# Kernel tuning notes

Hardware: AMD Instinct MI355X
Metric: run time of the kernel (lower is better)

## Reference

```python
import jax, jax.numpy as jnp
import numpy as np
import math

B, NB, NA, NC, D, E, H = 4, 2048, 1024, 1024, 1024, 8, 16
HD = D // H
TOP_K = 2
T_MAX = 1000.0
TAU_MIN, TAU_MAX = 0.5, 2.0
W_MIN, W_MAX = 0.1, 0.2
CAP_LO, CAP_HI = 0.5, 0.6
FLOOR = min(0.05, 0.15 / E)       # cfg.routing_floor property
ALPHA = min(FLOOR * E, 1.0)       # routing-floor interpolation weight
BIAS_COEFF = 0.01
EPS = 1e-8


def _layernorm(x, g, b, eps=1e-5):
    mu = x.mean(-1, keepdims=True)
    var = ((x - mu) ** 2).mean(-1, keepdims=True)
    return (x - mu) * jax.lax.rsqrt(var + eps) * g + b


def _forward(tokens_B, output_A, output_C, in_proj_w, in_proj_b, out_proj_w, out_proj_b,
             ln_g, ln_b, te_w1, te_b1, te_w2, te_b2,
             gate_w1, gate_b1, gate_w2, gate_b2, expert_bias, t):
    t_norm = t.astype(jnp.float32) / T_MAX                 # (B,)
    ctx_C = jax.lax.stop_gradient(output_C)                # stopgrad_C_to_B
    ctx_AC = jnp.concatenate([output_A, ctx_C], axis=1)    # (B, NA+NC, D)

    # --- cross attention (torch nn.MultiheadAttention, batch_first) ---
    wq, wk, wv = jnp.split(in_proj_w, 3, axis=0)
    bq, bk, bv = jnp.split(in_proj_b, 3)
    q = (tokens_B @ wq.T + bq).reshape(B, NB, H, HD)
    k = (ctx_AC @ wk.T + bk).reshape(B, NA + NC, H, HD)
    v = (ctx_AC @ wv.T + bv).reshape(B, NA + NC, H, HD)
    scores = jnp.einsum('bqhd,bkhd->bhqk', q, k) / math.sqrt(HD)
    attn = jax.nn.softmax(scores, axis=-1)
    ctx = jnp.einsum('bhqk,bkhd->bqhd', attn, v).reshape(B, NB, D)
    ctx_B = ctx @ out_proj_w.T + out_proj_b
    ctx_B = _layernorm(ctx_B + tokens_B, ln_g, ln_b)

    # --- sinusoidal timestep embedding + 2-layer MLP ---
    half = D // 2
    freq = jnp.exp(-math.log(10000.0) * jnp.arange(half, dtype=jnp.float32) / (half - 1))
    args = t.astype(jnp.float32)[:, None] * freq
    emb = jnp.concatenate([jnp.sin(args), jnp.cos(args)], axis=-1)   # (B, D)
    t_emb = jax.nn.silu(emb @ te_w1.T + te_b1) @ te_w2.T + te_b2     # (B, D)
    t_emb = jnp.broadcast_to(t_emb[:, None, :], (B, NB, D))

    # --- gate MLP + expert bias + temperature ---
    gate_in = jnp.concatenate([tokens_B, ctx_B, t_emb], axis=-1)     # (B, NB, 3D)
    logits = jax.nn.relu(gate_in @ gate_w1.T + gate_b1) @ gate_w2.T + gate_b2 + expert_bias
    tau = (TAU_MIN + (TAU_MAX - TAU_MIN) * t_norm)[:, None, None]
    probs = jax.nn.softmax(logits / tau, axis=-1)                    # (B, NB, E)

    # routing floor: interpolate toward uniform
    probs = (1.0 - ALPHA) * probs + ALPHA / E

    # shared expert injection: expert 0 gets scheduled weight w(t), rest renormalised
    w = (W_MIN + (W_MAX - W_MIN) * t_norm)[:, None, None]
    shared = jnp.maximum(probs[..., 0:1], w)
    others = probs[..., 1:]
    others = others / jnp.maximum(others.sum(-1, keepdims=True), EPS) * (1.0 - shared)
    probs = jnp.concatenate([shared, others], axis=-1)

    # top-k mask (keep top-k probs, zero the rest)
    vals, idx = jax.lax.top_k(probs, TOP_K)
    dispatch = (jax.nn.one_hot(idx, E, dtype=probs.dtype) * vals[..., None]).sum(-2)

    # token-level hard cap (torch.no_grad -> stop_gradient) with redistribution
    cap = (CAP_LO + (CAP_HI - CAP_LO) * t_norm)[:, None, None]
    excess = jax.nn.relu(dispatch - cap)
    capped = dispatch - excess
    headroom = jax.nn.relu(cap - capped)
    head_sum = jnp.maximum(headroom.sum(-1, keepdims=True), EPS)
    capped = capped + excess.sum(-1, keepdims=True) * (headroom / head_sum)
    dispatch = jax.lax.stop_gradient(capped)

    # batch-level utilisation penalty on specialists 1..E-1
    fair = NB / max(E - 1, 1)
    load = dispatch.sum(axis=1).mean(axis=0)                          # (E,)
    pen_excess = jax.nn.relu(load[1:] - fair * 1.5)
    bias_penalty = BIAS_COEFF * jnp.sum(pen_excess ** 2)

    combine = dispatch / (dispatch.sum(-1, keepdims=True) + EPS)
    return dispatch, combine, bias_penalty


def setup_inputs() -> dict:
    key = jax.random.key(0)
    ks = jax.random.split(key, 12)
    g = lambda k, sh: jax.random.normal(k, sh, jnp.float32) * 0.02
    return dict(
        tokens_B=jax.random.normal(ks[0], (B, NB, D), jnp.float32),
        output_A=jax.random.normal(ks[1], (B, NA, D), jnp.float32),
        output_C=jax.random.normal(ks[2], (B, NC, D), jnp.float32),
        t=jax.random.randint(ks[3], (B,), 0, 1000, jnp.int32),
        in_proj_w=g(ks[4], (3 * D, D)),
        in_proj_b=jnp.zeros((3 * D,), jnp.float32),
        out_proj_w=g(ks[5], (D, D)),
        out_proj_b=jnp.zeros((D,), jnp.float32),
        ln_g=jnp.ones((D,), jnp.float32),
        ln_b=jnp.zeros((D,), jnp.float32),
        te_w1=g(ks[6], (2 * D, D)),
        te_b1=jnp.zeros((2 * D,), jnp.float32),
        te_w2=g(ks[7], (D, 2 * D)),
        te_b2=jnp.zeros((D,), jnp.float32),
        gate_w1=g(ks[8], (D, 3 * D)),
        gate_b1=jnp.zeros((D,), jnp.float32),
        gate_w2=g(ks[9], (E, D)),
        gate_b2=jnp.zeros((E,), jnp.float32),
        expert_bias=jnp.zeros((E,), jnp.float32),
    )


def reference(tokens_B, output_A, output_C, t, in_proj_w, in_proj_b, out_proj_w, out_proj_b,
              ln_g, ln_b, te_w1, te_b1, te_w2, te_b2,
              gate_w1, gate_b1, gate_w2, gate_b2, expert_bias):
    return _forward(tokens_B, output_A, output_C, in_proj_w, in_proj_b, out_proj_w, out_proj_b,
                    ln_g, ln_b, te_w1, te_b1, te_w2, te_b2,
                    gate_w1, gate_b1, gate_w2, gate_b2, expert_bias, t)
```

## Files before the change

### kernel.cpp

```cpp
#include <hip/hip_runtime.h>
#include <math.h>


typedef __attribute__((ext_vector_type(8))) short short8;
typedef __attribute__((ext_vector_type(4))) float f32x4;
typedef __attribute__((ext_vector_type(4))) unsigned int u32x4;
typedef unsigned short u16;
typedef unsigned int u32;

__global__ void zero_k(double* p) {
    if (threadIdx.x < 8) p[threadIdx.x] = 0.0;
}

__device__ inline u16 bf_hi(float x) {
    u32 u = __float_as_uint(x);
    u += 0x7FFFu + ((u >> 16) & 1u);
    return (u16)(u >> 16);
}
__device__ inline u16 bf_lo(float x, u16 h) {
    float hf = __uint_as_float(((u32)h) << 16);
    return bf_hi(x - hf);
}
__device__ inline u32 pack_bf(float x) {
    u32 u = __float_as_uint(x);
    u32 hi = (u + (0x7FFFu + ((u >> 16) & 1u))) >> 16;
    float hf = __uint_as_float(hi << 16);
    float d = x - hf;
    u32 u2 = __float_as_uint(d);
    u32 lo = (u2 + (0x7FFFu + ((u2 >> 16) & 1u))) >> 16;
    return (hi << 16) | lo;
}

__device__ inline void pack2(float p0, float p1, u32& o0, u32& o1) {
    u32 h01, l01;
    asm("v_cvt_pk_bf16_f32 %0, %1, %2" : "=v"(h01) : "v"(p0), "v"(p1));
    float d0 = p0 - __uint_as_float(h01 << 16);
    float d1 = p1 - __uint_as_float(h01 & 0xffff0000u);
    asm("v_cvt_pk_bf16_f32 %0, %1, %2" : "=v"(l01) : "v"(d0), "v"(d1));
    o0 = __builtin_amdgcn_perm(h01, l01, 0x05040100u);
    o1 = __builtin_amdgcn_perm(h01, l01, 0x07060302u);
}

__global__ __launch_bounds__(256)
void split_k(const float* __restrict__ in, u16* __restrict__ hi,
             u16* __restrict__ lo, int n4) {
    int i = blockIdx.x * 256 + threadIdx.x;
    if (i >= n4) return;
    float4 x = ((const float4*)in)[i];
    ushort4 h, l;
    h.x = bf_hi(x.x); l.x = bf_lo(x.x, h.x);
    h.y = bf_hi(x.y); l.y = bf_lo(x.y, h.y);
    h.z = bf_hi(x.z); l.z = bf_lo(x.z, h.z);
    h.w = bf_hi(x.w); l.w = bf_lo(x.w, h.w);
    ((ushort4*)hi)[i] = h;
    ((ushort4*)lo)[i] = l;
}

__global__ void emb_k(const int* __restrict__ t, float* __restrict__ emb) {
    int b = blockIdx.x;
    int j = threadIdx.x;
    float x1 = (float)(-9.210340371976184) * (float)j;
    float x2 = x1 / 511.0f;
    float freq = (float)exp((double)x2);
    float tf = (float)t[b];
    float arg = tf * freq;
    emb[b * 1024 + j]       = (float)sin((double)arg);
    emb[b * 1024 + 512 + j] = (float)cos((double)arg);
}

__global__ void te_fc_k(const float* __restrict__ in, const float* __restrict__ W,
                        const float* __restrict__ bias, float* __restrict__ out,
                        int K, int N, int do_silu) {
    int b = blockIdx.x;
    int wv = threadIdx.x >> 6, lane = threadIdx.x & 63;
    const float* inb = in + (size_t)b * K;
    int n0 = blockIdx.y * 16 + wv * 4;
    for (int q = 0; q < 4; q++) {
        int n = n0 + q;
        const float* wr = W + (size_t)n * K;
        float acc = 0.f;
        for (int c = lane * 4; c < K; c += 256) {
            float4 a  = *(const float4*)(inb + c);
            float4 w4 = *(const float4*)(wr + c);
            acc += a.x * w4.x + a.y * w4.y + a.z * w4.z + a.w * w4.w;
        }
#pragma unroll
        for (int off = 1; off < 64; off <<= 1) acc += __shfl_xor(acc, off, 64);
        if (lane == 0) {
            float x = acc + bias[n];
            out[(size_t)b * N + n] = do_silu ? (x / (1.0f + expf(-x))) : x;
        }
    }
}

template<bool GATE, bool RELU, int OMODE>
__global__ __launch_bounds__(256, 2)
void bfgemm_k(const u16* __restrict__ A0h, const u16* __restrict__ A0l,
              const u16* __restrict__ A1h, const u16* __restrict__ A1l,
              const u16* __restrict__ A2h, const u16* __restrict__ A2l,
              const u16* __restrict__ Wh_g, const u16* __restrict__ Wl_g,
              const float* __restrict__ bias, float* __restrict__ C,
              u16* __restrict__ Chi, u16* __restrict__ Clo, int K, float scale)
{
    __shared__ u16 Ah[128 * 32];
    __shared__ u16 Al[128 * 32];
    __shared__ u16 Wh[128 * 32];
    __shared__ u16 Wl[128 * 32];
    const int tid = threadIdx.x;
    const int row0 = blockIdx.x * 128;
    const int col0 = blockIdx.y * 128;
    const int wv = tid >> 6;
    const int lane = tid & 63;
    const int wrow = (wv & 1) * 64;
    const int wcol = (wv >> 1) * 64;
    const int l15 = lane & 15, quad = lane >> 4;

    f32x4 acc[4][4];
#pragma unroll
    for (int i = 0; i < 4; i++)
#pragma unroll
        for (int j = 0; j < 4; j++)
            acc[i][j] = (f32x4){0.f, 0.f, 0.f, 0.f};

    const int ar0 = tid >> 2, ak0 = (tid & 3) * 8;
    const int ar1 = (tid + 256) >> 2, ak1 = ((tid + 256) & 3) * 8;

    for (int kc = 0; kc < K; kc += 32) {
        const u16* pAh = A0h;
        const u16* pAl = A0l;
        int kk = kc;
        int tembseg = 0;
        if (GATE) {
            int seg = kc >> 10;
            if (seg == 1) { pAh = A1h; pAl = A1l; }
            else if (seg == 2) { pAh = A2h; pAl = A2l; tembseg = 1; }
            kk = kc & 1023;
        }
        const int astr = GATE ? 1024 : K;
        int g0 = row0 + ar0, g1 = row0 + ar1;
        if (GATE && tembseg) { g0 >>= 11; g1 >>= 11; }
        uint4 vah0 = *(const uint4*)&pAh[(size_t)g0 * astr + kk + ak0];
        uint4 vah1 = *(const uint4*)&pAh[(size_t)g1 * astr + kk + ak1];
        uint4 val0 = *(const uint4*)&pAl[(size_t)g0 * astr + kk + ak0];
        uint4 val1 = *(const uint4*)&pAl[(size_t)g1 * astr + kk + ak1];
        uint4 vwh0 = *(const uint4*)&Wh_g[(size_t)(col0 + ar0) * K + kc + ak0];
        uint4 vwh1 = *(const uint4*)&Wh_g[(size_t)(col0 + ar1) * K + kc + ak1];
        uint4 vwl0 = *(const uint4*)&Wl_g[(size_t)(col0 + ar0) * K + kc + ak0];
        uint4 vwl1 = *(const uint4*)&Wl_g[(size_t)(col0 + ar1) * K + kc + ak1];
        __syncthreads();
        *(uint4*)&Ah[ar0 * 32 + ak0] = vah0;
        *(uint4*)&Ah[ar1 * 32 + ak1] = vah1;
        *(uint4*)&Al[ar0 * 32 + ak0] = val0;
        *(uint4*)&Al[ar1 * 32 + ak1] = val1;
        *(uint4*)&Wh[ar0 * 32 + ak0] = vwh0;
        *(uint4*)&Wh[ar1 * 32 + ak1] = vwh1;
        *(uint4*)&Wl[ar0 * 32 + ak0] = vwl0;
        *(uint4*)&Wl[ar1 * 32 + ak1] = vwl1;
        __syncthreads();

        short8 a_h[4], a_l[4];
#pragma unroll
        for (int i = 0; i < 4; i++) {
            int r = (wrow + i * 16 + l15) * 32 + quad * 8;
            a_h[i] = *(const short8*)&Ah[r];
            a_l[i] = *(const short8*)&Al[r];
        }
#pragma unroll
        for (int j = 0; j < 4; j++) {
            int c = (wcol + j * 16 + l15) * 32 + quad * 8;
            short8 b_h = *(const short8*)&Wh[c];
            short8 b_l = *(const short8*)&Wl[c];
#pragma unroll
            for (int i = 0; i < 4; i++) {
                acc[i][j] = __builtin_amdgcn_mfma_f32_16x16x32_bf16(a_h[i], b_h, acc[i][j], 0, 0, 0);
                acc[i][j] = __builtin_amdgcn_mfma_f32_16x16x32_bf16(a_h[i], b_l, acc[i][j], 0, 0, 0);
                acc[i][j] = __builtin_amdgcn_mfma_f32_16x16x32_bf16(a_l[i], b_h, acc[i][j], 0, 0, 0);
            }
        }
    }

#pragma unroll
    for (int i = 0; i < 4; i++) {
#pragma unroll
        for (int j = 0; j < 4; j++) {
            int cc = col0 + wcol + j * 16 + l15;
#pragma unroll
            for (int r = 0; r < 4; r++) {
                int rr = row0 + wrow + i * 16 + quad * 4 + r;
                float v = (acc[i][j][r] + ((OMODE == 3) ? bias[rr] : bias[cc])) * scale;
                if (RELU) v = fmaxf(v, 0.f);
                if (OMODE == 0) {
                    C[(size_t)rr * 1024 + cc] = v;
                } else if (OMODE == 1) {
                    u32 pk = pack_bf(v);
                    size_t a = (size_t)rr * 1024 + cc;
                    Chi[a] = (u16)(pk >> 16); Clo[a] = (u16)pk;
                } else if (OMODE == 2) {
                    int orow = ((rr >> 10) & 3) * 2048 + (rr >> 12) * 1024 + (rr & 1023);
                    u32 pk = pack_bf(v);
                    size_t a = (size_t)orow * 1024 + cc;
                    Chi[a] = (u16)(pk >> 16); Clo[a] = (u16)pk;
                } else {
                    int bb2 = (cc >> 10) & 3;
                    int key = (cc >> 12) * 1024 + (cc & 1023);
                    u32 pk = pack_bf(v);
                    size_t a = ((size_t)(bb2 * 1024 + rr)) * 2048 + key;
                    Chi[a] = (u16)(pk >> 16); Clo[a] = (u16)pk;
                }
            }
        }
    }
}

__global__ __launch_bounds__(512, 4)
void attn_k(const u16* Qh, const u16* Ql,
            const u16* __restrict__ Kh, const u16* __restrict__ Kl,
            const u16* __restrict__ Vh, const u16* __restrict__ Vl,
            u16* Oh, u16* Ol)
{
    __shared__ u32 Pu[256 * 64];
    __shared__ u16 Vsm[2][64 * 64];
    u16* Ksh = (u16*)Pu;
    u16* Ksl = Ksh + 64 * 64;

    const int tid = threadIdx.x;
    const int w = tid >> 6, lane = tid & 63;
    const int l15 = lane & 15, quad = lane >> 4;
    const int bh = blockIdx.x, b = bh >> 4, h = bh & 15;
    const int qw = blockIdx.y * 256 + w * 32;
    const int qrow0 = b * 2048 + qw;

    short8 qh_f[2][2], ql_f[2][2];
#pragma unroll
    for (int i = 0; i < 2; i++)
#pragma unroll
        for (int kc = 0; kc < 2; kc++) {
            size_t a = (size_t)(qrow0 + i * 16 + l15) * 1024 + h * 64 + kc * 32 + quad * 8;
            qh_f[i][kc] = *(const short8*)&Qh[a];
            ql_f[i][kc] = *(const short8*)&Ql[a];
        }

    const int skey = tid >> 3, sd8 = tid & 7;
    const int lds_kv = skey * 64 + ((sd8 ^ (skey & 7)) << 3);
    const size_t g_k = ((size_t)(b * 2048) + skey) * 1024 + h * 64 + sd8 * 8;
    const size_t g_v = ((size_t)((b * 16 + h) * 64 + skey)) * 2048 + sd8 * 8;

    uint4 pk_h = *(const uint4*)&Kh[g_k];
    uint4 pk_l = *(const uint4*)&Kl[g_k];
    uint4 pv_h = *(const uint4*)&Vh[g_v];
    uint4 pv_l = *(const uint4*)&Vl[g_v];

    f32x4 o[2][4];
#pragma unroll
    for (int i = 0; i < 2; i++)
#pragma unroll
        for (int j = 0; j < 4; j++) o[i][j] = (f32x4){0.f, 0.f, 0.f, 0.f};
    float lsum[2][4] = {};

    for (int kt = 0; kt < 32; kt++) {
        __syncthreads();
        *(uint4*)&Ksh[lds_kv] = pk_h;
        *(uint4*)&Ksl[lds_kv] = pk_l;
        *(uint4*)&Vsm[0][lds_kv] = pv_h;
        *(uint4*)&Vsm[1][lds_kv] = pv_l;
        __syncthreads();
        if (kt < 31) {
            size_t gk2 = g_k + (size_t)(kt + 1) * 65536;
            size_t gv2 = g_v + (size_t)(kt + 1) * 64;
            pk_h = *(const uint4*)&Kh[gk2];
            pk_l = *(const uint4*)&Kl[gk2];
            pv_h = *(const uint4*)&Vh[gv2];
            pv_l = *(const uint4*)&Vl[gv2];
        }
        f32x4 s[2][4];
#pragma unroll
        for (int i = 0; i < 2; i++)
#pragma unroll
            for (int j = 0; j < 4; j++) s[i][j] = (f32x4){0.f, 0.f, 0.f, 0.f};
#pragma unroll
        for (int j = 0; j < 4; j++) {
            int ka = (j * 16 + l15) * 64 + ((quad ^ (l15 & 7)) << 3);
            short8 kh0 = *(const short8*)&Ksh[ka];
            short8 kh1 = *(const short8*)&Ksh[ka ^ 32];
            short8 kl0 = *(const short8*)&Ksl[ka];
            short8 kl1 = *(const short8*)&Ksl[ka ^ 32];
#pragma unroll
            for (int i = 0; i < 2; i++) {
                s[i][j] = __builtin_amdgcn_mfma_f32_16x16x32_bf16(qh_f[i][0], kh0, s[i][j], 0, 0, 0);
                s[i][j] = __builtin_amdgcn_mfma_f32_16x16x32_bf16(qh_f[i][0], kl0, s[i][j], 0, 0, 0);
                s[i][j] = __builtin_amdgcn_mfma_f32_16x16x32_bf16(ql_f[i][0], kh0, s[i][j], 0, 0, 0);
                s[i][j] = __builtin_amdgcn_mfma_f32_16x16x32_bf16(qh_f[i][1], kh1, s[i][j], 0, 0, 0);
                s[i][j] = __builtin_amdgcn_mfma_f32_16x16x32_bf16(qh_f[i][1], kl1, s[i][j], 0, 0, 0);
                s[i][j] = __builtin_amdgcn_mfma_f32_16x16x32_bf16(ql_f[i][1], kh1, s[i][j], 0, 0, 0);
            }
        }
        __syncthreads();
#pragma unroll
        for (int i = 0; i < 2; i++)
#pragma unroll
            for (int j = 0; j < 4; j++) {
                float p0 = exp2f(s[i][j][0]);
                float p1 = exp2f(s[i][j][1]);
                float p2 = exp2f(s[i][j][2]);
                float p3 = exp2f(s[i][j][3]);
                lsum[i][0] += p0; lsum[i][1] += p1;
                lsum[i][2] += p2; lsum[i][3] += p3;
                u32 o0, o1, o2, o3;
                pack2(p0, p1, o0, o1);
                pack2(p2, p3, o2, o3);
                int rb = w * 32 + i * 16 + quad * 4;
                int csw = (j * 16 + l15) ^ ((i * 4 + quad) << 3);
                Pu[(rb + 0) * 64 + csw] = o0;
                Pu[(rb + 1) * 64 + csw] = o1;
                Pu[(rb + 2) * 64 + csw] = o2;
                Pu[(rb + 3) * 64 + csw] = o3;
            }
#pragma unroll
        for (int kc = 0; kc < 2; kc++) {
            short8 ph[2], pl[2];
#pragma unroll
            for (int i = 0; i < 2; i++) {
                int prow = w * 32 + i * 16 + l15;
                int pcol = (kc * 32 + quad * 8) ^ ((i * 4 + (l15 >> 2)) << 3);
                const uint4* pp = (const uint4*)&Pu[prow * 64 + pcol];
                uint4 u0 = pp[0], u1 = pp[1];
                union { short8 s; u32x4 u; } hh, ll;
                hh.u = (u32x4){ __builtin_amdgcn_perm(u0.y, u0.x, 0x07060302u),
                                __builtin_amdgcn_perm(u0.w, u0.z, 0x07060302u),
                                __builtin_amdgcn_perm(u1.y, u1.x, 0x07060302u),
                                __builtin_amdgcn_perm(u1.w, u1.z, 0x07060302u) };
                ll.u = (u32x4){ __builtin_amdgcn_perm(u0.y, u0.x, 0x05040100u),
                                __builtin_amdgcn_perm(u0.w, u0.z, 0x05040100u),
                                __builtin_amdgcn_perm(u1.y, u1.x, 0x05040100u),
                                __builtin_amdgcn_perm(u1.w, u1.z, 0x05040100u) };
                ph[i] = hh.s; pl[i] = ll.s;
            }
#pragma unroll
            for (int jd = 0; jd < 4; jd++) {
                int va = (jd * 16 + l15) * 64 + ((((kc << 2) + quad) ^ (l15 & 7)) << 3);
                short8 vvh = *(const short8*)&Vsm[0][va];
                short8 vvl = *(const short8*)&Vsm[1][va];
#pragma unroll
                for (int i = 0; i < 2; i++) {
                    o[i][jd] = __builtin_amdgcn_mfma_f32_16x16x32_bf16(ph[i], vvh, o[i][jd], 0, 0, 0);
                    o[i][jd] = __builtin_amdgcn_mfma_f32_16x16x32_bf16(ph[i], vvl, o[i][jd], 0, 0, 0);
                    o[i][jd] = __builtin_amdgcn_mfma_f32_16x16x32_bf16(pl[i], vvh, o[i][jd], 0, 0, 0);
                }
            }
        }
    }
#pragma unroll
    for (int i = 0; i < 2; i++)
#pragma unroll
        for (int r = 0; r < 4; r++) {
            float s2 = lsum[i][r];
            s2 += __shfl_xor(s2, 1, 64);
            s2 += __shfl_xor(s2, 2, 64);
            s2 += __shfl_xor(s2, 4, 64);
            s2 += __shfl_xor(s2, 8, 64);
            lsum[i][r] = s2;
        }
#pragma unroll
    for (int i = 0; i < 2; i++)
#pragma unroll
        for (int jd = 0; jd < 4; jd++)
#pragma unroll
            for (int r = 0; r < 4; r++) {
                float v = o[i][jd][r] / lsum[i][r];
                u32 pk = pack_bf(v);
                size_t a = (size_t)(qrow0 + i * 16 + quad * 4 + r) * 1024 + h * 64 + jd * 16 + l15;
                Oh[a] = (u16)(pk >> 16);
                Ol[a] = (u16)pk;
            }
}

__global__ __launch_bounds__(256)
void ln_split_k(const float* __restrict__ X, const float* __restrict__ T,
                const float* __restrict__ g, const float* __restrict__ bta,
                u16* __restrict__ chi, u16* __restrict__ clo)
{
    __shared__ float red[8];
    int r = blockIdx.x, tid = threadIdx.x;
    size_t base = (size_t)r * 1024 + tid * 4;
    float4 x  = *(const float4*)(X + base);
    float4 tk = *(const float4*)(T + base);
    x.x += tk.x; x.y += tk.y; x.z += tk.z; x.w += tk.w;
    float s = x.x + x.y + x.z + x.w;
#pragma unroll
    for (int off = 1; off < 64; off <<= 1) s += __shfl_xor(s, off, 64);
    int wv = tid >> 6;
    if ((tid & 63) == 0) red[wv] = s;
    __syncthreads();
    float mu = (red[0] + red[1] + red[2] + red[3]) * (1.0f / 1024.0f);
    float dx0 = x.x - mu, dx1 = x.y - mu, dx2 = x.z - mu, dx3 = x.w - mu;
    float ss = dx0 * dx0 + dx1 * dx1 + dx2 * dx2 + dx3 * dx3;
#pragma unroll
    for (int off = 1; off < 64; off <<= 1) ss += __shfl_xor(ss, off, 64);
    if ((tid & 63) == 0) red[4 + wv] = ss;
    __syncthreads();
    float var = (red[4] + red[5] + red[6] + red[7]) * (1.0f / 1024.0f);
    float inv = 1.0f / sqrtf(var + 1e-5f);
    float4 gg = *(const float4*)(g + tid * 4);
    float4 bb = *(const float4*)(bta + tid * 4);
    float y0 = dx0 * inv * gg.x + bb.x;
    float y1 = dx1 * inv * gg.y + bb.y;
    float y2 = dx2 * inv * gg.z + bb.z;
    float y3 = dx3 * inv * gg.w + bb.w;
    ushort4 h, l;
    h.x = bf_hi(y0); l.x = bf_lo(y0, h.x);
    h.y = bf_hi(y1); l.y = bf_lo(y1, h.y);
    h.z = bf_hi(y2); l.z = bf_lo(y2, h.z);
    h.w = bf_hi(y3); l.w = bf_lo(y3, h.w);
    *(ushort4*)&chi[base] = h;
    *(ushort4*)&clo[base] = l;
}

__global__ __launch_bounds__(256)
void logits_k(const float* __restrict__ Hd, const float* __restrict__ W2,
              const float* __restrict__ b2, const float* __restrict__ eb,
              float* __restrict__ Lg)
{
    int gw = (blockIdx.x * 256 + threadIdx.x) >> 6;
    int lane = threadIdx.x & 63;
    const float* h = Hd + (size_t)gw * 1024;
    float4 hv[4];
#pragma unroll
    for (int j = 0; j < 4; j++) hv[j] = *(const float4*)(h + j * 256 + lane * 4);
    float res[8];
#pragma unroll
    for (int e = 0; e < 8; e++) {
        const float* w = W2 + (size_t)e * 1024;
        float acc = 0.f;
#pragma unroll
        for (int j = 0; j < 4; j++) {
            float4 w4 = *(const float4*)(w + j * 256 + lane * 4);
            acc += hv[j].x * w4.x + hv[j].y * w4.y + hv[j].z * w4.z + hv[j].w * w4.w;
        }
#pragma unroll
        for (int off = 1; off < 64; off <<= 1) acc += __shfl_xor(acc, off, 64);
        res[e] = acc;
    }
    if (lane < 8) {
        float v = res[0];
#pragma unroll
        for (int e = 1; e < 8; e++) v = (lane == e) ? res[e] : v;
        Lg[(size_t)gw * 8 + lane] = v + b2[lane] + eb[lane];
    }
}

__global__ __launch_bounds__(256)
void router_k(const float* __restrict__ Lg, const int* __restrict__ t,
              float* __restrict__ outp, double* __restrict__ loadAcc)
{
    __shared__ double wred[4][8];
    int tid = threadIdx.x;
    int r = blockIdx.x * 256 + tid;
    int b = r >> 11;
    float tn  = (float)t[b] / 1000.0f;
    float tau = 0.5f + 1.5f * tn;
    float p[8];
    float mx = -INFINITY;
#pragma unroll
    for (int e = 0; e < 8; e++) { p[e] = Lg[(size_t)r * 8 + e] / tau; mx = fmaxf(mx, p[e]); }
    float sum = 0.f;
#pragma unroll
    for (int e = 0; e < 8; e++) { p[e] = expf(p[e] - mx); sum += p[e]; }
#pragma unroll
    for (int e = 0; e < 8; e++) p[e] = p[e] / sum;
#pragma unroll
    for (int e = 0; e < 8; e++) p[e] = 0.85f * p[e] + 0.01875f;
    float w = 0.1f + 0.1f * tn;
    float shared_p = fmaxf(p[0], w);
    float osum = 0.f;
#pragma unroll
    for (int e = 1; e < 8; e++) osum += p[e];
    float denom_o = fmaxf(osum, 1e-8f);
    float one_m = 1.0f - shared_p;
    p[0] = shared_p;
#pragma unroll
    for (int e = 1; e < 8; e++) p[e] = (p[e] / denom_o) * one_m;
    int i0 = 0; float v0 = p[0];
#pragma unroll
    for (int e = 1; e < 8; e++) if (p[e] > v0) { v0 = p[e]; i0 = e; }
    int i1 = -1; float v1 = -INFINITY;
#pragma unroll
    for (int e = 0; e < 8; e++) if (e != i0 && p[e] > v1) { v1 = p[e]; i1 = e; }
    float cap = 0.5f + 0.1f * tn;
    float dsp[8], capped[8], hr[8];
    float exsum = 0.f, hsum = 0.f;
#pragma unroll
    for (int e = 0; e < 8; e++) {
        float d = ((e == i0) ? v0 : 0.f) + ((e == i1) ? v1 : 0.f);
        float ex = fmaxf(d - cap, 0.f);
        float c = d - ex;
        float hh = fmaxf(cap - c, 0.f);
        capped[e] = c; hr[e] = hh;
        exsum += ex; hsum += hh;
    }
    float hden = fmaxf(hsum, 1e-8f);
    float dsum = 0.f;
#pragma unroll
    for (int e = 0; e < 8; e++) {
        float d = capped[e] + exsum * (hr[e] / hden);
        dsp[e] = d; dsum += d;
    }
    float cden = dsum + 1e-8f;
#pragma unroll
    for (int e = 0; e < 8; e++) {
        outp[(size_t)r * 8 + e] = dsp[e];
        outp[65536 + (size_t)r * 8 + e] = dsp[e] / cden;
    }
    int lane = tid & 63, wv = tid >> 6;
#pragma unroll
    for (int e = 0; e < 8; e++) {
        double s = (double)dsp[e];
#pragma unroll
        for (int off = 1; off < 64; off <<= 1) s += __shfl_xor(s, off, 64);
        if (lane == 0) wred[wv][e] = s;
    }
    __syncthreads();
    if (tid < 8) {
        double s = wred[0][tid] + wred[1][tid] + wred[2][tid] + wred[3][tid];
        atomicAdd(&loadAcc[tid], s);
    }
}

__global__ void penalty_k(const double* __restrict__ loadAcc, float* __restrict__ outp) {
    if (threadIdx.x == 0) {
        const float thr = (float)(2048.0 / 7.0 * 1.5);
        float pen = 0.f;
#pragma unroll
        for (int e = 1; e < 8; e++) {
            float load = (float)(loadAcc[e] / 4.0);
            float x = fmaxf(load - thr, 0.f);
            pen += x * x;
        }
        outp[131072] = 0.01f * pen;
    }
}

extern "C" void kernel_launch(void* const* d_in, const int* in_sizes, int n_in,
                              void* d_out, int out_size, void* d_ws, size_t ws_size,
                              hipStream_t stream)
{
    const float* tokens = (const float*)d_in[0];
    const float* outA   = (const float*)d_in[1];
    const float* outC   = (const float*)d_in[2];
    const int*   tt     = (const int*)  d_in[3];
    const float* in_w   = (const float*)d_in[4];
    const float* in_b   = (const float*)d_in[5];
    const float* op_w   = (const float*)d_in[6];
    const float* op_b   = (const float*)d_in[7];
    const float* lng    = (const float*)d_in[8];
    const float* lnb    = (const float*)d_in[9];
    const float* te_w1  = (const float*)d_in[10];
    const float* te_b1  = (const float*)d_in[11];
    const float* te_w2  = (const float*)d_in[12];
    const float* te_b2  = (const float*)d_in[13];
    const float* g_w1   = (const float*)d_in[14];
    const float* g_b1   = (const float*)d_in[15];
    const float* g_w2   = (const float*)d_in[16];
    const float* g_b2   = (const float*)d_in[17];
    const float* e_bias = (const float*)d_in[18];
    float* out = (float*)d_out;

    float* ws = (float*)d_ws;
    const size_t NM = (size_t)8192 * 1024;
    float* F0     = ws;
    float* temb   = ws + NM;
    float* embb   = temb + 4096;
    float* hte    = embb + 4096;
    float* logitsb = hte + 8192;
    double* loads = (double*)(logitsb + 65536);

    u16* U = (u16*)(loads + 16);
    u16* Tokh = U;
    u16* Tokl = Tokh + NM;
    u16* ActH = Tokl + NM;
    u16* ActL = ActH + NM;
    u16* Qh   = ActL + NM;
    u16* Ql   = Qh + NM;
    u16* Kh   = Ql + NM;
    u16* Kl   = Kh + NM;
    u16* Vth  = Kl + NM;
    u16* Vtl  = Vth + NM;
    u16* Wsh  = Vtl + NM;
    u16* Wsl  = Wsh + (size_t)3 * 1024 * 1024;
    u16* Tbh  = Wsl + (size_t)3 * 1024 * 1024;
    u16* Tbl  = Tbh + 4096;

    zero_k<<<1, 64, 0, stream>>>(loads);
    emb_k<<<4, 512, 0, stream>>>(tt, embb);
    te_fc_k<<<dim3(4, 128), 256, 0, stream>>>(embb, te_w1, te_b1, hte, 1024, 2048, 1);
    te_fc_k<<<dim3(4, 64),  256, 0, stream>>>(hte,  te_w2, te_b2, temb, 2048, 1024, 0);

    split_k<<<8192, 256, 0, stream>>>(tokens, Tokh, Tokl, 8192 * 1024 / 4);
    split_k<<<3072, 256, 0, stream>>>(in_w, Wsh, Wsl, 3 * 1024 * 1024 / 4);
    split_k<<<4096, 256, 0, stream>>>(outA, ActH, ActL, 4096 * 1024 / 4);
    split_k<<<4096, 256, 0, stream>>>(outC, ActH + (size_t)4096 * 1024,
                                      ActL + (size_t)4096 * 1024, 4096 * 1024 / 4);

    bfgemm_k<false, false, 1><<<dim3(64, 8), 256, 0, stream>>>(
        Tokh, Tokl, nullptr, nullptr, nullptr, nullptr,
        Wsh, Wsl, in_b, nullptr, Qh, Ql, 1024, 0.18033688011112042f);
    bfgemm_k<false, false, 2><<<dim3(64, 8), 256, 0, stream>>>(
        ActH, ActL, nullptr, nullptr, nullptr, nullptr,
        Wsh + (size_t)1024 * 1024, Wsl + (size_t)1024 * 1024,
        in_b + 1024, nullptr, Kh, Kl, 1024, 1.0f);
    bfgemm_k<false, false, 3><<<dim3(8, 64), 256, 0, stream>>>(
        Wsh + (size_t)2048 * 1024, Wsl + (size_t)2048 * 1024,
        nullptr, nullptr, nullptr, nullptr,
        ActH, ActL, in_b + 2048, nullptr, Vth, Vtl, 1024, 1.0f);

    attn_k<<<dim3(64, 8), 512, 0, stream>>>(Qh, Ql, Kh, Kl, Vth, Vtl, Qh, Ql);

    split_k<<<1024, 256, 0, stream>>>(op_w, Wsh, Wsl, 1024 * 1024 / 4);
    bfgemm_k<false, false, 0><<<dim3(64, 8), 256, 0, stream>>>(
        Qh, Ql, nullptr, nullptr, nullptr, nullptr,
        Wsh, Wsl, op_b, F0, nullptr, nullptr, 1024, 1.0f);

    ln_split_k<<<8192, 256, 0, stream>>>(F0, tokens, lng, lnb, Kh, Kl);

    split_k<<<4, 256, 0, stream>>>(temb, Tbh, Tbl, 4096 / 4);
    split_k<<<3072, 256, 0, stream>>>(g_w1, Wsh, Wsl, 3072 * 1024 / 4);
    bfgemm_k<true, true, 0><<<dim3(64, 8), 256, 0, stream>>>(
        Tokh, Tokl, Kh, Kl, Tbh, Tbl,
        Wsh, Wsl, g_b1, F0, nullptr, nullptr, 3072, 1.0f);

    logits_k<<<2048, 256, 0, stream>>>(F0, g_w2, g_b2, e_bias, logitsb);
    router_k<<<32, 256, 0, stream>>>(logitsb, tt, out, loads);
    penalty_k<<<1, 64, 0, stream>>>(loads, out);
}
```

Baseline: 1.007 ms.

## Stream attention K/V tiles straight into LDS and halve the attention block size

Result: faster. 859.0 us (-14.7%).

```diff
diff --git a/kernel.cpp b/kernel.cpp
--- a/kernel.cpp
+++ b/kernel.cpp
@@ -39,6 +39,13 @@
     asm("v_cvt_pk_bf16_f32 %0, %1, %2" : "=v"(l01) : "v"(d0), "v"(d1));
     o0 = __builtin_amdgcn_perm(h01, l01, 0x05040100u);
     o1 = __builtin_amdgcn_perm(h01, l01, 0x07060302u);
+}
+
+__device__ inline void async16(const u16* g, u16* l) {
+    __builtin_amdgcn_global_load_lds(
+        (const __attribute__((address_space(1))) unsigned int*)g,
+        (__attribute__((address_space(3))) unsigned int*)l,
+        16, 0, 0);
 }
 
 __global__ __launch_bounds__(256)
@@ -212,13 +219,13 @@
     }
 }
 
-__global__ __launch_bounds__(512, 4)
+__global__ __launch_bounds__(256)
 void attn_k(const u16* Qh, const u16* Ql,
             const u16* __restrict__ Kh, const u16* __restrict__ Kl,
             const u16* __restrict__ Vh, const u16* __restrict__ Vl,
             u16* Oh, u16* Ol)
 {
-    __shared__ u32 Pu[256 * 64];
+    __shared__ u32 Pu[128 * 64];
     __shared__ u16 Vsm[2][64 * 64];
     u16* Ksh = (u16*)Pu;
     u16* Ksl = Ksh + 64 * 64;
@@ -227,7 +234,7 @@
     const int w = tid >> 6, lane = tid & 63;
     const int l15 = lane & 15, quad = lane >> 4;
     const int bh = blockIdx.x, b = bh >> 4, h = bh & 15;
-    const int qw = blockIdx.y * 256 + w * 32;
+    const int qw = blockIdx.y * 128 + w * 32;
     const int qrow0 = b * 2048 + qw;
 
     short8 qh_f[2][2], ql_f[2][2];
@@ -240,15 +247,12 @@
             ql_f[i][kc] = *(const short8*)&Ql[a];
         }
 
-    const int skey = tid >> 3, sd8 = tid & 7;
-    const int lds_kv = skey * 64 + ((sd8 ^ (skey & 7)) << 3);
-    const size_t g_k = ((size_t)(b * 2048) + skey) * 1024 + h * 64 + sd8 * 8;
-    const size_t g_v = ((size_t)((b * 16 + h) * 64 + skey)) * 2048 + sd8 * 8;
-
-    uint4 pk_h = *(const uint4*)&Kh[g_k];
-    uint4 pk_l = *(const uint4*)&Kl[g_k];
-    uint4 pv_h = *(const uint4*)&Vh[g_v];
-    uint4 pv_l = *(const uint4*)&Vl[g_v];
+    const int srow = tid >> 3;
+    const int scsw = ((tid & 7) ^ (srow & 7)) << 3;
+    const size_t gk_base = ((size_t)(b * 2048) + srow) * 1024 + h * 64 + scsw;
+    const size_t gv_base = ((size_t)((b * 16 + h) * 64 + srow)) * 2048 + scsw;
+    u16* ldsK = Ksh + w * 512;
+    u16* ldsV = &Vsm[0][0] + w * 512;
 
     f32x4 o[2][4];
 #pragma unroll
@@ -259,19 +263,19 @@
 
     for (int kt = 0; kt < 32; kt++) {
         __syncthreads();
-        *(uint4*)&Ksh[lds_kv] = pk_h;
-        *(uint4*)&Ksl[lds_kv] = pk_l;
-        *(uint4*)&Vsm[0][lds_kv] = pv_h;
-        *(uint4*)&Vsm[1][lds_kv] = pv_l;
+        {
+            const size_t gk = gk_base + (size_t)kt * 65536;
+            const size_t gv = gv_base + (size_t)kt * 64;
+            async16(&Kh[gk],         ldsK);
+            async16(&Kh[gk + 32768], ldsK + 2048);
+            async16(&Kl[gk],         ldsK + 4096);
+            async16(&Kl[gk + 32768], ldsK + 6144);
+            async16(&Vh[gv],         ldsV);
+            async16(&Vh[gv + 65536], ldsV + 2048);
+            async16(&Vl[gv],         ldsV + 4096);
+            async16(&Vl[gv + 65536], ldsV + 6144);
+        }
         __syncthreads();
-        if (kt < 31) {
-            size_t gk2 = g_k + (size_t)(kt + 1) * 65536;
-            size_t gv2 = g_v + (size_t)(kt + 1) * 64;
-            pk_h = *(const uint4*)&Kh[gk2];
-            pk_l = *(const uint4*)&Kl[gk2];
-            pv_h = *(const uint4*)&Vh[gv2];
-            pv_l = *(const uint4*)&Vl[gv2];
-        }
         f32x4 s[2][4];
 #pragma unroll
         for (int i = 0; i < 2; i++)
@@ -612,7 +616,7 @@
         nullptr, nullptr, nullptr, nullptr,
         ActH, ActL, in_b + 2048, nullptr, Vth, Vtl, 1024, 1.0f);
 
-    attn_k<<<dim3(64, 8), 512, 0, stream>>>(Qh, Ql, Kh, Kl, Vth, Vtl, Qh, Ql);
+    attn_k<<<dim3(64, 16), 256, 0, stream>>>(Qh, Ql, Kh, Kl, Vth, Vtl, Qh, Ql);
 
     split_k<<<1024, 256, 0, stream>>>(op_w, Wsh, Wsl, 1024 * 1024 / 4);
     bfgemm_k<false, false, 0><<<dim3(64, 8), 256, 0, stream>>>(
```
